# Optimization experiments

Hardware: AMD Instinct MI355X
Metric: run time of the kernel (lower is better)

The kernel has to match this reference:

```python
import jax, jax.numpy as jnp
import numpy as np

N = 500_000   # points
V = 65_536    # voxels
C_IN = 6
GF = 64
OUT = 256


def setup_inputs() -> dict:
    key = jax.random.key(0)
    ks = jax.random.split(key, 14)
    p = lambda k, shape: (jax.random.normal(k, shape, jnp.float32) * 0.05)
    return {
        "inp_feat": jax.random.normal(ks[0], (N, C_IN), jnp.float32),
        "vox2point_idx": jax.random.randint(ks[1], (N,), 0, V, jnp.int64),
        "W1": p(ks[2], (C_IN, GF)),        "b1": p(ks[3], (GF,)),
        "W2": p(ks[4], (GF, OUT // 2)),    "b2": p(ks[5], (OUT // 2,)),
        "Wv1": p(ks[6], (OUT // 2, OUT // 2)), "bv1": p(ks[7], (OUT // 2,)),
        "W3": p(ks[8], (OUT, OUT)),        "b3": p(ks[9], (OUT,)),
        "W4": p(ks[10], (OUT, OUT)),       "b4": p(ks[11], (OUT,)),
        "Wv2": p(ks[12], (OUT, OUT)),      "bv2": p(ks[13], (OUT,)),
    }


def _segment_max0(x, idx, num_segments):
    # torch_scatter scatter(..., reduce='max') initializes empty slots to 0
    s = jax.ops.segment_max(x, idx, num_segments=num_segments)
    return jnp.where(jnp.isfinite(s), s, jnp.zeros((), x.dtype))


def reference(inp_feat, vox2point_idx, W1, b1, W2, b2, Wv1, bv1, W3, b3, W4, b4, Wv2, bv2):
    relu = jax.nn.relu
    point_feat1 = relu(inp_feat @ W1 + b1)            # [N, 64]
    point_feat2 = relu(point_feat1 @ W2 + b2)         # [N, 128]
    occ_voxel_feat = _segment_max0(point_feat2, vox2point_idx, V)   # [V, 128]
    occ_voxel_feat = relu(occ_voxel_feat @ Wv1 + bv1)               # [V, 128]
    point_global_feat = occ_voxel_feat[vox2point_idx]               # [N, 128] gather
    point_feat3 = jnp.concatenate([point_global_feat, point_feat2], axis=-1)  # [N, 256]
    point_feat4 = relu(point_feat3 @ W3 + b3)         # [N, 256]
    point_feat5 = relu(point_feat4 @ W4 + b4)         # [N, 256]
    occ_voxel_feat2 = _segment_max0(point_feat5, vox2point_idx, V)  # [V, 256]
    occ_voxel_feat2 = relu(occ_voxel_feat2 @ Wv2 + bv2)             # [V, 256]
    return occ_voxel_feat2
```

## Files before the change

### kernel.cpp

```cpp
#include <hip/hip_runtime.h>
#include <hip/hip_bf16.h>
#include <stdint.h>

#define N_PTS 500000
#define NVOX  65536
#define K1_TILES ((N_PTS + 127) / 128)
#define K3_TILES ((N_PTS + 63) / 64)

typedef __attribute__((ext_vector_type(8))) short bf16x8;
typedef __attribute__((ext_vector_type(4))) float f32x4;

__device__ inline unsigned short f2bf(float f) {
    union { float f; unsigned int u; } v; v.f = f;
    unsigned int r = v.u + 0x7FFFu + ((v.u >> 16) & 1u);
    return (unsigned short)(r >> 16);
}
__device__ inline float bf2f(unsigned short h) {
    return __uint_as_float((unsigned int)h << 16);
}

#define WOFF_W1T   0
#define WOFF_W2T   2048
#define WOFF_WV1T  10240
#define WOFF_W3AT  26624
#define WOFF_W3BT  59392
#define WOFF_W4T   92160
#define WOFF_WV2T  157696
#define W_TOTAL    223232

__global__ void prep_all(const float* __restrict__ W1, const float* __restrict__ W2,
                         const float* __restrict__ Wv1, const float* __restrict__ W3,
                         const float* __restrict__ W4, const float* __restrict__ Wv2,
                         unsigned short* __restrict__ dst) {
    int i = blockIdx.x * 256 + threadIdx.x;
    if (i >= W_TOTAL) return;
    int o = i;
    if (o < 2048) {
        int n = o >> 5, k = o & 31;
        dst[i] = (k < 6) ? f2bf(W1[k * 64 + n]) : (unsigned short)0;
    } else if ((o -= 2048) < 8192) {
        int n = o >> 6, k = o & 63;
        dst[i] = f2bf(W2[k * 128 + n]);
    } else if ((o -= 8192) < 16384) {
        int n = o >> 7, k = o & 127;
        dst[i] = f2bf(Wv1[k * 128 + n]);
    } else if ((o -= 16384) < 32768) {
        int n = o >> 7, k = o & 127;
        dst[i] = f2bf(W3[k * 256 + n]);
    } else if ((o -= 32768) < 32768) {
        int n = o >> 7, k = o & 127;
        dst[i] = f2bf(W3[(k + 128) * 256 + n]);
    } else if ((o -= 32768) < 65536) {
        int n = o >> 8, k = o & 255;
        dst[i] = f2bf(W4[k * 256 + n]);
    } else {
        o -= 65536;
        int n = o >> 8, k = o & 255;
        dst[i] = f2bf(Wv2[k * 256 + n]);
    }
}

__global__ void s_hist(const int* __restrict__ idx, unsigned int* __restrict__ counts) {
    int p = blockIdx.x * 256 + threadIdx.x;
    if (p < N_PTS) atomicAdd(&counts[idx[p]], 1u);
}

__global__ __launch_bounds__(1024) void s_scan(const unsigned int* __restrict__ counts,
                                               unsigned int* __restrict__ cursor) {
    __shared__ unsigned int sPart[1024];
    int t = threadIdx.x;
    unsigned int sum = 0;
    #pragma unroll 8
    for (int i = 0; i < 64; i++) sum += counts[t * 64 + i];
    sPart[t] = sum;
    __syncthreads();
    for (int d = 1; d < 1024; d <<= 1) {
        unsigned int add = (t >= d) ? sPart[t - d] : 0u;
        __syncthreads();
        sPart[t] += add;
        __syncthreads();
    }
    unsigned int run = (t == 0) ? 0u : sPart[t - 1];
    #pragma unroll 8
    for (int i = 0; i < 64; i++) {
        cursor[t * 64 + i] = run;
        run += counts[t * 64 + i];
    }
}

__global__ void s_scatter(const int* __restrict__ idx, unsigned int* __restrict__ cursor,
                          int* __restrict__ order, int* __restrict__ svox) {
    int p = blockIdx.x * 256 + threadIdx.x;
    if (p < N_PTS) {
        int v = idx[p];
        unsigned int pos = atomicAdd(&cursor[v], 1u);
        order[pos] = p;
        svox[pos] = v;
    }
}

__global__ __launch_bounds__(256) void k1_points(
    const float* __restrict__ inp,
    const int* __restrict__ order, const int* __restrict__ svox,
    const unsigned short* __restrict__ W1T, const float* __restrict__ b1,
    const unsigned short* __restrict__ W2T, const float* __restrict__ b2,
    unsigned int* __restrict__ vox1acc)
{
    __shared__ __align__(16) char sBuf[32 * 1024];
    __shared__ float sb1[64];
    __shared__ float sb2[128];
    __shared__ int   sVox[128];
    char* sIn = sBuf;
    char* sF1 = sBuf + 8 * 1024;
    char* sF2 = sBuf;
    const f32x4 fzero = {0.f, 0.f, 0.f, 0.f};
    int tid = threadIdx.x;
    int pbase = blockIdx.x * 128;
    if (tid < 64)       sb1[tid] = b1[tid];
    else if (tid < 192) sb2[tid - 64] = b2[tid - 64];
    if (tid < 128) {
        int i = pbase + tid;
        int pt = -1, v = -1;
        if (i < N_PTS) { pt = order[i]; v = svox[i]; }
        sVox[tid] = v;
        uint4 g0 = {0u, 0u, 0u, 0u};
        if (pt >= 0) {
            const float* x = inp + (size_t)pt * 6;
            g0.x = (unsigned)f2bf(x[0]) | ((unsigned)f2bf(x[1]) << 16);
            g0.y = (unsigned)f2bf(x[2]) | ((unsigned)f2bf(x[3]) << 16);
            g0.z = (unsigned)f2bf(x[4]) | ((unsigned)f2bf(x[5]) << 16);
        }
        int swz = (tid & 3) << 4;
        char* row = sIn + tid * 64;
        uint4 z = {0u, 0u, 0u, 0u};
        *(uint4*)(row + (0  ^ swz)) = g0;
        *(uint4*)(row + (16 ^ swz)) = z;
        *(uint4*)(row + (32 ^ swz)) = z;
        *(uint4*)(row + (48 ^ swz)) = z;
    }
    __syncthreads();
    int wave = tid >> 6, lane = tid & 63, quad = lane >> 4, l16 = lane & 15;

    {
        f32x4 acc1[8];
        #pragma unroll
        for (int mt = 0; mt < 8; mt++) acc1[mt] = fzero;
        int n = wave * 16 + l16;
        bf16x8 b = *(const bf16x8*)(W1T + n * 32 + quad * 8);
        #pragma unroll
        for (int mt = 0; mt < 8; mt++) {
            int m = mt * 16 + l16;
            bf16x8 a = *(const bf16x8*)(sIn + m * 64 + ((quad * 16) ^ ((m & 3) << 4)));
            acc1[mt] = __builtin_amdgcn_mfma_f32_16x16x32_bf16(a, b, acc1[mt], 0, 0, 0);
        }
        float bias = sb1[n];
        #pragma unroll
        for (int mt = 0; mt < 8; mt++)
            #pragma unroll
            for (int r = 0; r < 4; r++) {
                int m = mt * 16 + quad * 4 + r;
                float v = fmaxf(acc1[mt][r] + bias, 0.f);
                *(unsigned short*)(sF1 + m * 128 + ((2 * n) ^ ((m & 7) << 4))) = f2bf(v);
            }
    }
    __syncthreads();
    f32x4 acc2[2][8];
    #pragma unroll
    for (int j = 0; j < 2; j++)
        #pragma unroll
        for (int mt = 0; mt < 8; mt++) acc2[j][mt] = fzero;
    #pragma unroll
    for (int kt = 0; kt < 2; kt++) {
        bf16x8 b0 = *(const bf16x8*)(W2T + ((wave * 2 + 0) * 16 + l16) * 64 + kt * 32 + quad * 8);
        bf16x8 b1 = *(const bf16x8*)(W2T + ((wave * 2 + 1) * 16 + l16) * 64 + kt * 32 + quad * 8);
        #pragma unroll
        for (int mt = 0; mt < 8; mt++) {
            int m = mt * 16 + l16;
            bf16x8 a = *(const bf16x8*)(sF1 + m * 128 + ((kt * 64 + quad * 16) ^ ((m & 7) << 4)));
            acc2[0][mt] = __builtin_amdgcn_mfma_f32_16x16x32_bf16(a, b0, acc2[0][mt], 0, 0, 0);
            acc2[1][mt] = __builtin_amdgcn_mfma_f32_16x16x32_bf16(a, b1, acc2[1][mt], 0, 0, 0);
        }
    }
    __syncthreads();
    #pragma unroll
    for (int j = 0; j < 2; j++) {
        int n = (wave * 2 + j) * 16 + l16;
        float bias = sb2[n];
        #pragma unroll
        for (int mt = 0; mt < 8; mt++)
            #pragma unroll
            for (int r = 0; r < 4; r++) {
                int m = mt * 16 + quad * 4 + r;
                float v = fmaxf(acc2[j][mt][r] + bias, 0.f);
                *(unsigned short*)(sF2 + m * 256 + ((2 * n) ^ ((m & 7) << 4))) = f2bf(v);
            }
    }
    __syncthreads();
    {
        int c = tid & 127, r0 = (tid >> 7) * 64;
        int cur = -1; float vmax = 0.f; int segStart = r0;
        for (int r = r0; r < r0 + 64; r++) {
            int v = sVox[r];
            float f = bf2f(*(const unsigned short*)(sF2 + r * 256 + ((2 * c) ^ ((r & 7) << 4))));
            if (v != cur) {
                if (cur >= 0) {
                    if (segStart > r0)
                        vox1acc[(size_t)cur * 128 + c] = __float_as_uint(vmax);
                    else
                        atomicMax(vox1acc + (size_t)cur * 128 + c, __float_as_uint(vmax));
                }
                cur = v; vmax = f; segStart = r;
            } else vmax = fmaxf(vmax, f);
        }
        if (cur >= 0)
            atomicMax(vox1acc + (size_t)cur * 128 + c, __float_as_uint(vmax));
    }
}

__global__ __launch_bounds__(256) void kvox2(
    const float* __restrict__ in, const unsigned short* __restrict__ Wv1T,
    const float* __restrict__ bv1, const unsigned short* __restrict__ W3aT,
    unsigned short* __restrict__ voxB)
{
    __shared__ __align__(16) char sA[64 * 256];
    __shared__ __align__(16) char sB[64 * 256];
    __shared__ float sb[128];
    const f32x4 fzero = {0.f, 0.f, 0.f, 0.f};
    int tid = threadIdx.x;
    int vb = blockIdx.x * 64;
    if (tid < 128) sb[tid] = bv1[tid];
    #pragma unroll
    for (int it = 0; it < 8; it++) {
        int i = tid + 256 * it;
        int m = i >> 5, kq = i & 31;
        float4 f = ((const float4*)(in + (size_t)(vb + m) * 128))[kq];
        uint2 p;
        p.x = (unsigned)f2bf(f.x) | ((unsigned)f2bf(f.y) << 16);
        p.y = (unsigned)f2bf(f.z) | ((unsigned)f2bf(f.w) << 16);
        *(uint2*)(sA + m * 256 + ((8 * kq) ^ ((m & 7) << 4))) = p;
    }
    __syncthreads();
    int wave = tid >> 6, lane = tid & 63, quad = lane >> 4, l16 = lane & 15;
    {
        f32x4 acc[2][4];
        #pragma unroll
        for (int j = 0; j < 2; j++)
            #pragma unroll
            for (int mt = 0; mt < 4; mt++) acc[j][mt] = fzero;
        #pragma unroll
        for (int kt = 0; kt < 4; kt++) {
            bf16x8 a[4];
            #pragma unroll
            for (int mt = 0; mt < 4; mt++) {
                int m = mt * 16 + l16;
                a[mt] = *(const bf16x8*)(sA + m * 256 + ((kt * 64 + quad * 16) ^ ((m & 7) << 4)));
            }
            #pragma unroll
            for (int j = 0; j < 2; j++) {
                int n = (wave * 2 + j) * 16 + l16;
                bf16x8 b = *(const bf16x8*)(Wv1T + n * 128 + kt * 32 + quad * 8);
                #pragma unroll
                for (int mt = 0; mt < 4; mt++)
                    acc[j][mt] = __builtin_amdgcn_mfma_f32_16x16x32_bf16(a[mt], b, acc[j][mt], 0, 0, 0);
            }
        }
        #pragma unroll
        for (int j = 0; j < 2; j++) {
            int n = (wave * 2 + j) * 16 + l16;
            float bi = sb[n];
            #pragma unroll
            for (int mt = 0; mt < 4; mt++)
                #pragma unroll
                for (int r = 0; r < 4; r++) {
                    int m = mt * 16 + quad * 4 + r;
                    float v = fmaxf(acc[j][mt][r] + bi, 0.f);
                    *(unsigned short*)(sB + m * 256 + ((2 * n) ^ ((m & 7) << 4))) = f2bf(v);
                }
        }
    }
    __syncthreads();
    {
        f32x4 acc[4][4];
        #pragma unroll
        for (int j = 0; j < 4; j++)
            #pragma unroll
            for (int mt = 0; mt < 4; mt++) acc[j][mt] = fzero;
        #pragma unroll
        for (int kt = 0; kt < 4; kt++) {
            bf16x8 a[4];
            #pragma unroll
            for (int mt = 0; mt < 4; mt++) {
                int m = mt * 16 + l16;
                a[mt] = *(const bf16x8*)(sB + m * 256 + ((kt * 64 + quad * 16) ^ ((m & 7) << 4)));
            }
            #pragma unroll
            for (int j = 0; j < 4; j++) {
                int n = (wave * 4 + j) * 16 + l16;
                bf16x8 b = *(const bf16x8*)(W3aT + n * 128 + kt * 32 + quad * 8);
                #pragma unroll
                for (int mt = 0; mt < 4; mt++)
                    acc[j][mt] = __builtin_amdgcn_mfma_f32_16x16x32_bf16(a[mt], b, acc[j][mt], 0, 0, 0);
            }
        }
        #pragma unroll
        for (int j = 0; j < 4; j++) {
            int n = (wave * 4 + j) * 16 + l16;
            #pragma unroll
            for (int mt = 0; mt < 4; mt++)
                #pragma unroll
                for (int r = 0; r < 4; r++) {
                    int m = mt * 16 + quad * 4 + r;
                    voxB[(size_t)(vb + m) * 256 + n] = f2bf(acc[j][mt][r]);
                }
        }
    }
}

__global__ __launch_bounds__(256, 3) void k3_heavy(
    const float* __restrict__ inp,
    const int* __restrict__ order, const int* __restrict__ svox,
    const unsigned short* __restrict__ W1T, const float* __restrict__ b1,
    const unsigned short* __restrict__ W2T, const float* __restrict__ b2,
    const unsigned short* __restrict__ voxB,
    const unsigned short* __restrict__ W3bT, const float* __restrict__ b3,
    const unsigned short* __restrict__ W4T, const float* __restrict__ b4,
    unsigned int* __restrict__ vox2acc)
{
    __shared__ __align__(16) char sBuf[32 * 1024];
    __shared__ float sb1[64];
    __shared__ float sb2[128];
    __shared__ float sb3[256];
    __shared__ float sb4[256];
    __shared__ int   sVox[64];
    char* sF2 = sBuf;
    char* sF1 = sBuf + 16 * 1024;
    char* sIn = sBuf + 24 * 1024;
    char* sP  = sBuf;
    const f32x4 fzero = {0.f, 0.f, 0.f, 0.f};
    int tid = threadIdx.x;
    int pbase = blockIdx.x * 64;
    sb3[tid] = b3[tid];
    sb4[tid] = b4[tid];
    if (tid < 64)  sb1[tid] = b1[tid];
    if (tid < 128) sb2[tid] = b2[tid];
    if (tid < 64) {
        int i = pbase + tid;
        int pt = -1, v = -1;
        if (i < N_PTS) { pt = order[i]; v = svox[i]; }
        sVox[tid] = v;
        uint4 g0 = {0u, 0u, 0u, 0u};
        if (pt >= 0) {
            const float* x = inp + (size_t)pt * 6;
            g0.x = (unsigned)f2bf(x[0]) | ((unsigned)f2bf(x[1]) << 16);
            g0.y = (unsigned)f2bf(x[2]) | ((unsigned)f2bf(x[3]) << 16);
            g0.z = (unsigned)f2bf(x[4]) | ((unsigned)f2bf(x[5]) << 16);
        }
        int swz = (tid & 3) << 4;
        char* row = sIn + tid * 64;
        uint4 z = {0u, 0u, 0u, 0u};
        *(uint4*)(row + (0  ^ swz)) = g0;
        *(uint4*)(row + (16 ^ swz)) = z;
        *(uint4*)(row + (32 ^ swz)) = z;
        *(uint4*)(row + (48 ^ swz)) = z;
    }
    __syncthreads();
    int wave = tid >> 6, lane = tid & 63, quad = lane >> 4, l16 = lane & 15;

    {
        f32x4 acc1[4];
        #pragma unroll
        for (int mt = 0; mt < 4; mt++) acc1[mt] = fzero;
        int n = wave * 16 + l16;
        bf16x8 b = *(const bf16x8*)(W1T + n * 32 + quad * 8);
        #pragma unroll
        for (int mt = 0; mt < 4; mt++) {
            int m = mt * 16 + l16;
            bf16x8 a = *(const bf16x8*)(sIn + m * 64 + ((quad * 16) ^ ((m & 3) << 4)));
            acc1[mt] = __builtin_amdgcn_mfma_f32_16x16x32_bf16(a, b, acc1[mt], 0, 0, 0);
        }
        float bias = sb1[n];
        #pragma unroll
        for (int mt = 0; mt < 4; mt++)
            #pragma unroll
            for (int r = 0; r < 4; r++) {
                int m = mt * 16 + quad * 4 + r;
                float v = fmaxf(acc1[mt][r] + bias, 0.f);
                *(unsigned short*)(sF1 + m * 128 + ((2 * n) ^ ((m & 7) << 4))) = f2bf(v);
            }
    }
    __syncthreads();
    {
        f32x4 acc2[2][4];
        #pragma unroll
        for (int j = 0; j < 2; j++)
            #pragma unroll
            for (int mt = 0; mt < 4; mt++) acc2[j][mt] = fzero;
        #pragma unroll
        for (int kt = 0; kt < 2; kt++) {
            bf16x8 b0 = *(const bf16x8*)(W2T + ((wave * 2 + 0) * 16 + l16) * 64 + kt * 32 + quad * 8);
            bf16x8 b1 = *(const bf16x8*)(W2T + ((wave * 2 + 1) * 16 + l16) * 64 + kt * 32 + quad * 8);
            #pragma unroll
            for (int mt = 0; mt < 4; mt++) {
                int m = mt * 16 + l16;
                bf16x8 a = *(const bf16x8*)(sF1 + m * 128 + ((kt * 64 + quad * 16) ^ ((m & 7) << 4)));
                acc2[0][mt] = __builtin_amdgcn_mfma_f32_16x16x32_bf16(a, b0, acc2[0][mt], 0, 0, 0);
                acc2[1][mt] = __builtin_amdgcn_mfma_f32_16x16x32_bf16(a, b1, acc2[1][mt], 0, 0, 0);
            }
        }
        #pragma unroll
        for (int j = 0; j < 2; j++) {
            int n = (wave * 2 + j) * 16 + l16;
            float bias = sb2[n];
            #pragma unroll
            for (int mt = 0; mt < 4; mt++)
                #pragma unroll
                for (int r = 0; r < 4; r++) {
                    int m = mt * 16 + quad * 4 + r;
                    float v = fmaxf(acc2[j][mt][r] + bias, 0.f);
                    *(unsigned short*)(sF2 + m * 256 + ((2 * n) ^ ((m & 7) << 4))) = f2bf(v);
                }
        }
    }
    __syncthreads();

    f32x4 acc[4][4];
    #pragma unroll
    for (int j = 0; j < 4; j++)
        #pragma unroll
        for (int mt = 0; mt < 4; mt++) acc[j][mt] = fzero;
    #pragma unroll 1
    for (int kt = 0; kt < 4; kt++) {
        bf16x8 a[4];
        #pragma unroll
        for (int mt = 0; mt < 4; mt++) {
            int m = mt * 16 + l16;
            a[mt] = *(const bf16x8*)(sF2 + m * 256 + ((kt * 64 + quad * 16) ^ ((m & 7) << 4)));
        }
        #pragma unroll
        for (int j = 0; j < 4; j++) {
            int n = (wave * 4 + j) * 16 + l16;
            bf16x8 b = *(const bf16x8*)(W3bT + n * 128 + kt * 32 + quad * 8);
            #pragma unroll
            for (int mt = 0; mt < 4; mt++)
                acc[j][mt] = __builtin_amdgcn_mfma_f32_16x16x32_bf16(a[mt], b, acc[j][mt], 0, 0, 0);
        }
    }
    __syncthreads();
    #pragma unroll
    for (int it = 0; it < 8; it++) {
        int i = tid + 256 * it;
        int m = i >> 5, c = i & 31;
        int vv = sVox[m];
        uint4 val = {0u, 0u, 0u, 0u};
        if (vv >= 0)
            val = ((const uint4*)(voxB + (size_t)vv * 256))[c];
        *(uint4*)(sP + m * 512 + ((c * 16) ^ ((m & 7) << 4))) = val;
    }
    __syncthreads();
    #pragma unroll
    for (int j = 0; j < 4; j++) {
        int n = (wave * 4 + j) * 16 + l16;
        float bias = sb3[n];
        #pragma unroll
        for (int mt = 0; mt < 4; mt++)
            #pragma unroll
            for (int r = 0; r < 4; r++) {
                int m = mt * 16 + quad * 4 + r;
                char* p = sP + m * 512 + ((2 * n) ^ ((m & 7) << 4));
                float vox = bf2f(*(const unsigned short*)p);
                float v = fmaxf(acc[j][mt][r] + bias + vox, 0.f);
                *(unsigned short*)p = f2bf(v);
            }
    }
    __syncthreads();
    #pragma unroll
    for (int j = 0; j < 4; j++)
        #pragma unroll
        for (int mt = 0; mt < 4; mt++) acc[j][mt] = fzero;
    #pragma unroll 1
    for (int kt = 0; kt < 8; kt++) {
        bf16x8 a[4];
        #pragma unroll
        for (int mt = 0; mt < 4; mt++) {
            int m = mt * 16 + l16;
            a[mt] = *(const bf16x8*)(sP + m * 512 + ((kt * 64 + quad * 16) ^ ((m & 7) << 4)));
        }
        #pragma unroll
        for (int j = 0; j < 4; j++) {
            int n = (wave * 4 + j) * 16 + l16;
            bf16x8 b = *(const bf16x8*)(W4T + n * 256 + kt * 32 + quad * 8);
            #pragma unroll
            for (int mt = 0; mt < 4; mt++)
                acc[j][mt] = __builtin_amdgcn_mfma_f32_16x16x32_bf16(a[mt], b, acc[j][mt], 0, 0, 0);
        }
    }
    __syncthreads();
    #pragma unroll
    for (int j = 0; j < 4; j++) {
        int n = (wave * 4 + j) * 16 + l16;
        float bias = sb4[n];
        #pragma unroll
        for (int mt = 0; mt < 4; mt++)
            #pragma unroll
            for (int r = 0; r < 4; r++) {
                int m = mt * 16 + quad * 4 + r;
                float v = fmaxf(acc[j][mt][r] + bias, 0.f);
                *(unsigned short*)(sP + m * 512 + ((2 * n) ^ ((m & 7) << 4))) = f2bf(v);
            }
    }
    __syncthreads();
    {
        int c = tid;
        int cur = -1; float vmax = 0.f; int segStart = 0;
        for (int r = 0; r < 64; r++) {
            int v = sVox[r];
            float f = bf2f(*(const unsigned short*)(sP + r * 512 + ((2 * c) ^ ((r & 7) << 4))));
            if (v != cur) {
                if (cur >= 0) {
                    if (segStart > 0)
                        vox2acc[(size_t)cur * 256 + c] = __float_as_uint(vmax);
                    else
                        atomicMax(vox2acc + (size_t)cur * 256 + c, __float_as_uint(vmax));
                }
                cur = v; vmax = f; segStart = r;
            } else vmax = fmaxf(vmax, f);
        }
        if (cur >= 0)
            atomicMax(vox2acc + (size_t)cur * 256 + c, __float_as_uint(vmax));
    }
}

__global__ __launch_bounds__(256) void kvox_final(
    const float* __restrict__ in, const unsigned short* __restrict__ WT,
    const float* __restrict__ bias, float* __restrict__ outp)
{
    __shared__ __align__(16) char sA[64 * 512];
    __shared__ float sb[256];
    const f32x4 fzero = {0.f, 0.f, 0.f, 0.f};
    int tid = threadIdx.x;
    int vb = blockIdx.x * 64;
    sb[tid] = bias[tid];
    #pragma unroll
    for (int it = 0; it < 16; it++) {
        int i = tid + 256 * it;
        int m = i >> 6, kq = i & 63;
        float4 f = ((const float4*)(in + (size_t)(vb + m) * 256))[kq];
        uint2 p;
        p.x = (unsigned)f2bf(f.x) | ((unsigned)f2bf(f.y) << 16);
        p.y = (unsigned)f2bf(f.z) | ((unsigned)f2bf(f.w) << 16);
        *(uint2*)(sA + m * 512 + ((8 * kq) ^ ((m & 7) << 4))) = p;
    }
    __syncthreads();
    int wave = tid >> 6, lane = tid & 63, quad = lane >> 4, l16 = lane & 15;
    f32x4 acc[4][4];
    #pragma unroll
    for (int j = 0; j < 4; j++)
        #pragma unroll
        for (int mt = 0; mt < 4; mt++) acc[j][mt] = fzero;
    #pragma unroll 1
    for (int kt = 0; kt < 8; kt++) {
        bf16x8 a[4];
        #pragma unroll
        for (int mt = 0; mt < 4; mt++) {
            int m = mt * 16 + l16;
            a[mt] = *(const bf16x8*)(sA + m * 512 + ((kt * 64 + quad * 16) ^ ((m & 7) << 4)));
        }
        #pragma unroll
        for (int j = 0; j < 4; j++) {
            int n = (wave * 4 + j) * 16 + l16;
            bf16x8 b = *(const bf16x8*)(WT + n * 256 + kt * 32 + quad * 8);
            #pragma unroll
            for (int mt = 0; mt < 4; mt++)
                acc[j][mt] = __builtin_amdgcn_mfma_f32_16x16x32_bf16(a[mt], b, acc[j][mt], 0, 0, 0);
        }
    }
    #pragma unroll
    for (int j = 0; j < 4; j++) {
        int n = (wave * 4 + j) * 16 + l16;
        float bi = sb[n];
        #pragma unroll
        for (int mt = 0; mt < 4; mt++)
            #pragma unroll
            for (int r = 0; r < 4; r++) {
                int m = mt * 16 + quad * 4 + r;
                outp[(size_t)(vb + m) * 256 + n] = fmaxf(acc[j][mt][r] + bi, 0.f);
            }
    }
}

extern "C" void kernel_launch(void* const* d_in, const int* in_sizes, int n_in,
                              void* d_out, int out_size, void* d_ws, size_t ws_size,
                              hipStream_t stream) {
    const float* inp  = (const float*)d_in[0];
    const int*   idx  = (const int*)d_in[1];
    const float* W1   = (const float*)d_in[2];
    const float* b1   = (const float*)d_in[3];
    const float* W2   = (const float*)d_in[4];
    const float* b2   = (const float*)d_in[5];
    const float* Wv1  = (const float*)d_in[6];
    const float* bv1  = (const float*)d_in[7];
    const float* W3   = (const float*)d_in[8];
    const float* b3   = (const float*)d_in[9];
    const float* W4   = (const float*)d_in[10];
    const float* b4   = (const float*)d_in[11];
    const float* Wv2  = (const float*)d_in[12];
    const float* bv2  = (const float*)d_in[13];

    char* ws = (char*)d_ws;
    size_t off = 0;
    unsigned int*   vox1acc = (unsigned int*)(ws + off);   off += (size_t)NVOX * 128 * 4;
    unsigned int*   counts  = (unsigned int*)(ws + off);   off += (size_t)NVOX * 4;
    unsigned int*   cursor  = (unsigned int*)(ws + off);   off += (size_t)NVOX * 4;
    int*            order   = (int*)(ws + off);            off += (size_t)N_PTS * 4;
    int*            svox    = (int*)(ws + off);            off += (size_t)N_PTS * 4;
    unsigned short* wsW     = (unsigned short*)(ws + off); off += (size_t)W_TOTAL * 2;

    const unsigned short* W1T  = wsW + WOFF_W1T;
    const unsigned short* W2T  = wsW + WOFF_W2T;
    const unsigned short* Wv1T = wsW + WOFF_WV1T;
    const unsigned short* W3aT = wsW + WOFF_W3AT;
    const unsigned short* W3bT = wsW + WOFF_W3BT;
    const unsigned short* W4T  = wsW + WOFF_W4T;
    const unsigned short* Wv2T = wsW + WOFF_WV2T;

    unsigned short* voxB = (unsigned short*)vox1acc;
    unsigned int* vox2acc = (unsigned int*)d_out;

    hipMemsetAsync(vox1acc, 0, (size_t)NVOX * 128 * 4 + (size_t)NVOX * 4, stream);
    hipMemsetAsync(vox2acc, 0, (size_t)NVOX * 256 * 4, stream);

    prep_all<<<(W_TOTAL + 255) / 256, 256, 0, stream>>>(W1, W2, Wv1, W3, W4, Wv2, wsW);

    s_hist<<<(N_PTS + 255) / 256, 256, 0, stream>>>(idx, counts);
    s_scan<<<1, 1024, 0, stream>>>(counts, cursor);
    s_scatter<<<(N_PTS + 255) / 256, 256, 0, stream>>>(idx, cursor, order, svox);

    k1_points<<<K1_TILES, 256, 0, stream>>>(inp, order, svox, W1T, b1, W2T, b2, vox1acc);
    kvox2<<<NVOX / 64, 256, 0, stream>>>((const float*)vox1acc, Wv1T, bv1, W3aT, voxB);
    k3_heavy<<<K3_TILES, 256, 0, stream>>>(inp, order, svox, W1T, b1, W2T, b2, voxB,
                                           W3bT, b3, W4T, b4, vox2acc);
    kvox_final<<<NVOX / 64, 256, 0, stream>>>((const float*)vox2acc, Wv2T, bv2,
                                              (float*)d_out);
}
```

Measured before the change: 661.0 us.

## Cache sorted point_feat2 from k1 and skip recompute in new k3_lite kernel

```diff
diff --git a/kernel.cpp b/kernel.cpp
--- a/kernel.cpp
+++ b/kernel.cpp
@@ -104,7 +104,8 @@
     const int* __restrict__ order, const int* __restrict__ svox,
     const unsigned short* __restrict__ W1T, const float* __restrict__ b1,
     const unsigned short* __restrict__ W2T, const float* __restrict__ b2,
-    unsigned int* __restrict__ vox1acc)
+    unsigned int* __restrict__ vox1acc,
+    unsigned short* __restrict__ feat2seq)
 {
     __shared__ __align__(16) char sBuf[32 * 1024];
     __shared__ float sb1[64];
@@ -196,6 +197,17 @@
             }
     }
     __syncthreads();
+    if (feat2seq) {
+        #pragma unroll
+        for (int it = 0; it < 8; it++) {
+            int i = tid + 256 * it;
+            int m = i >> 4, q = i & 15;
+            if (pbase + m < N_PTS) {
+                uint4 val = *(const uint4*)(sF2 + m * 256 + ((q * 16) ^ ((m & 7) << 4)));
+                *(uint4*)(feat2seq + (size_t)(pbase + m) * 128 + q * 8) = val;
+            }
+        }
+    }
     {
         int c = tid & 127, r0 = (tid >> 7) * 64;
         int cur = -1; float vmax = 0.f; int segStart = r0;
@@ -313,6 +325,148 @@
                     voxB[(size_t)(vb + m) * 256 + n] = f2bf(acc[j][mt][r]);
                 }
         }
+    }
+}
+
+__global__ __launch_bounds__(256, 3) void k3_lite(
+    const int* __restrict__ svox,
+    const unsigned short* __restrict__ feat2seq,
+    const unsigned short* __restrict__ voxB,
+    const unsigned short* __restrict__ W3bT, const float* __restrict__ b3,
+    const unsigned short* __restrict__ W4T, const float* __restrict__ b4,
+    unsigned int* __restrict__ vox2acc)
+{
+    __shared__ __align__(16) char sBuf[48 * 1024];
+    __shared__ float sb3[256];
+    __shared__ float sb4[256];
+    __shared__ int   sVox[64];
+    char* sP  = sBuf;
+    char* sF2 = sBuf + 32 * 1024;
+    const f32x4 fzero = {0.f, 0.f, 0.f, 0.f};
+    int tid = threadIdx.x;
+    int pbase = blockIdx.x * 64;
+    sb3[tid] = b3[tid];
+    sb4[tid] = b4[tid];
+    if (tid < 64) {
+        int i = pbase + tid;
+        sVox[tid] = (i < N_PTS) ? svox[i] : -1;
+    }
+    #pragma unroll
+    for (int it = 0; it < 4; it++) {
+        int i = tid + 256 * it;
+        int m = i >> 4, q = i & 15;
+        uint4 val = {0u, 0u, 0u, 0u};
+        if (pbase + m < N_PTS)
+            val = ((const uint4*)(feat2seq + (size_t)(pbase + m) * 128))[q];
+        *(uint4*)(sF2 + m * 256 + ((q * 16) ^ ((m & 7) << 4))) = val;
+    }
+    #pragma unroll
+    for (int it = 0; it < 8; it++) {
+        int i = tid + 256 * it;
+        int m = i >> 5, c = i & 31;
+        uint4 val = {0u, 0u, 0u, 0u};
+        int p = pbase + m;
+        if (p < N_PTS) {
+            int vv = svox[p];
+            val = ((const uint4*)(voxB + (size_t)vv * 256))[c];
+        }
+        *(uint4*)(sP + m * 512 + ((c * 16) ^ ((m & 7) << 4))) = val;
+    }
+    __syncthreads();
+    int wave = tid >> 6, lane = tid & 63, quad = lane >> 4, l16 = lane & 15;
+
+    f32x4 acc[4][4];
+    #pragma unroll
+    for (int j = 0; j < 4; j++)
+        #pragma unroll
+        for (int mt = 0; mt < 4; mt++) acc[j][mt] = fzero;
+    #pragma unroll 1
+    for (int kt = 0; kt < 4; kt++) {
+        bf16x8 a[4];
+        #pragma unroll
+        for (int mt = 0; mt < 4; mt++) {
+            int m = mt * 16 + l16;
+            a[mt] = *(const bf16x8*)(sF2 + m * 256 + ((kt * 64 + quad * 16) ^ ((m & 7) << 4)));
+        }
+        #pragma unroll
+        for (int j = 0; j < 4; j++) {
+            int n = (wave * 4 + j) * 16 + l16;
+            bf16x8 b = *(const bf16x8*)(W3bT + n * 128 + kt * 32 + quad * 8);
+            #pragma unroll
+            for (int mt = 0; mt < 4; mt++)
+                acc[j][mt] = __builtin_amdgcn_mfma_f32_16x16x32_bf16(a[mt], b, acc[j][mt], 0, 0, 0);
+        }
+    }
+    #pragma unroll
+    for (int j = 0; j < 4; j++) {
+        int n = (wave * 4 + j) * 16 + l16;
+        float bias = sb3[n];
+        #pragma unroll
+        for (int mt = 0; mt < 4; mt++)
+            #pragma unroll
+            for (int r = 0; r < 4; r++) {
+                int m = mt * 16 + quad * 4 + r;
+                char* p = sP + m * 512 + ((2 * n) ^ ((m & 7) << 4));
+                float vox = bf2f(*(const unsigned short*)p);
+                float v = fmaxf(acc[j][mt][r] + bias + vox, 0.f);
+                *(unsigned short*)p = f2bf(v);
+            }
+    }
+    __syncthreads();
+    #pragma unroll
+    for (int j = 0; j < 4; j++)
+        #pragma unroll
+        for (int mt = 0; mt < 4; mt++) acc[j][mt] = fzero;
+    #pragma unroll 1
+    for (int kt = 0; kt < 8; kt++) {
+        bf16x8 a[4];
+        #pragma unroll
+        for (int mt = 0; mt < 4; mt++) {
+            int m = mt * 16 + l16;
+            a[mt] = *(const bf16x8*)(sP + m * 512 + ((kt * 64 + quad * 16) ^ ((m & 7) << 4)));
+        }
+        #pragma unroll
+        for (int j = 0; j < 4; j++) {
+            int n = (wave * 4 + j) * 16 + l16;
+            bf16x8 b = *(const bf16x8*)(W4T + n * 256 + kt * 32 + quad * 8);
+            #pragma unroll
+            for (int mt = 0; mt < 4; mt++)
+                acc[j][mt] = __builtin_amdgcn_mfma_f32_16x16x32_bf16(a[mt], b, acc[j][mt], 0, 0, 0);
+        }
+    }
+    __syncthreads();
+    #pragma unroll
+    for (int j = 0; j < 4; j++) {
+        int n = (wave * 4 + j) * 16 + l16;
+        float bias = sb4[n];
+        #pragma unroll
+        for (int mt = 0; mt < 4; mt++)
+            #pragma unroll
+            for (int r = 0; r < 4; r++) {
+                int m = mt * 16 + quad * 4 + r;
+                float v = fmaxf(acc[j][mt][r] + bias, 0.f);
+                *(unsigned short*)(sP + m * 512 + ((2 * n) ^ ((m & 7) << 4))) = f2bf(v);
+            }
+    }
+    __syncthreads();
+    {
+        int c = tid;
+        int cur = -1; float vmax = 0.f; int segStart = 0;
+        for (int r = 0; r < 64; r++) {
+            int v = sVox[r];
+            float f = bf2f(*(const unsigned short*)(sP + r * 512 + ((2 * c) ^ ((r & 7) << 4))));
+            if (v != cur) {
+                if (cur >= 0) {
+                    if (segStart > 0)
+                        vox2acc[(size_t)cur * 256 + c] = __float_as_uint(vmax);
+                    else
+                        atomicMax(vox2acc + (size_t)cur * 256 + c, __float_as_uint(vmax));
+                }
+                cur = v; vmax = f; segStart = r;
+            } else vmax = fmaxf(vmax, f);
+        }
+        if (cur >= 0)
+            atomicMax(vox2acc + (size_t)cur * 256 + c, __float_as_uint(vmax));
     }
 }
 
@@ -615,6 +769,10 @@
     int*            svox    = (int*)(ws + off);            off += (size_t)N_PTS * 4;
     unsigned short* wsW     = (unsigned short*)(ws + off); off += (size_t)W_TOTAL * 2;
 
+    unsigned short* feat2seq = nullptr;
+    if (ws_size >= off + (size_t)N_PTS * 128 * 2)
+        feat2seq = (unsigned short*)(ws + off);
+
     const unsigned short* W1T  = wsW + WOFF_W1T;
     const unsigned short* W2T  = wsW + WOFF_W2T;
     const unsigned short* Wv1T = wsW + WOFF_WV1T;
@@ -635,10 +793,15 @@
     s_scan<<<1, 1024, 0, stream>>>(counts, cursor);
     s_scatter<<<(N_PTS + 255) / 256, 256, 0, stream>>>(idx, cursor, order, svox);
 
-    k1_points<<<K1_TILES, 256, 0, stream>>>(inp, order, svox, W1T, b1, W2T, b2, vox1acc);
+    k1_points<<<K1_TILES, 256, 0, stream>>>(inp, order, svox, W1T, b1, W2T, b2,
+                                            vox1acc, feat2seq);
     kvox2<<<NVOX / 64, 256, 0, stream>>>((const float*)vox1acc, Wv1T, bv1, W3aT, voxB);
-    k3_heavy<<<K3_TILES, 256, 0, stream>>>(inp, order, svox, W1T, b1, W2T, b2, voxB,
-                                           W3bT, b3, W4T, b4, vox2acc);
+    if (feat2seq)
+        k3_lite<<<K3_TILES, 256, 0, stream>>>(svox, feat2seq, voxB,
+                                              W3bT, b3, W4T, b4, vox2acc);
+    else
+        k3_heavy<<<K3_TILES, 256, 0, stream>>>(inp, order, svox, W1T, b1, W2T, b2, voxB,
+                                               W3bT, b3, W4T, b4, vox2acc);
     kvox_final<<<NVOX / 64, 256, 0, stream>>>((const float*)vox2acc, Wv2T, bv2,
                                               (float*)d_out);
 }
```

New measurement: 648.1 us. Within noise of the previous version (-1.9%).
